# Kernel tuning notes

Measured on AMD Instinct MI355X. Metric: run time of the kernel, lower is better.

## Reference

```python
import jax, jax.numpy as jnp
import numpy as np

B, T, D, K = 8, 2048, 128, 2


def setup_inputs() -> dict:
    key = jax.random.key(0)
    k1, k2 = jax.random.split(key)
    z = jax.random.normal(k1, (B, T, D), dtype=jnp.float32)
    gt_dT = jax.random.normal(k2, (B, T, T, K), dtype=jnp.float32)
    sigma = jnp.ones((K,), dtype=jnp.float32)
    return {"z": z, "gt_dT": gt_dT, "sigma": sigma}


def reference(z, gt_dT, sigma):
    # z: [B,T,D], gt_dT: [B,T,T,K], sigma: [K]
    two_sigma_sq = 2.0 * sigma * sigma                    # [K]
    kernel = jnp.sum(gt_dT * gt_dT / two_sigma_sq, axis=-1)  # [B,T,T]
    w = jnp.exp(-kernel)                                  # [B,T,T]
    z2 = jnp.einsum('btd,btd->bt', z, z)                  # [B,T] squared norms
    w_row_col_sum = jnp.sum(w, axis=2) + jnp.sum(w, axis=1)  # [B,T]
    term1_plus_3 = jnp.einsum('bt,bt->b', z2, w_row_col_sum)  # [B]
    wz = jnp.einsum('bij,bjd->bid', w, z)                 # [B,T,D]
    term2 = jnp.einsum('bid,bid->b', wz, z)               # [B]
    Tn = z.shape[1]
    loss = jnp.mean(term1_plus_3 - 2.0 * term2) / (Tn * Tn)
    return loss
```

## Files before the change

### kernel.cpp

```cpp
#include <hip/hip_runtime.h>


#define T_DIM 2048
#define D_DIM 128
#define B_DIM 8
#define TILE 64
#define NTHREADS 256
#define LDS_STRIDE 136

typedef short s16x8 __attribute__((ext_vector_type(8)));
typedef float f32x4 __attribute__((ext_vector_type(4)));

__device__ __forceinline__ unsigned short f2bf(float x) {
    unsigned int u = __float_as_uint(x);
    u += 0x7fffu + ((u >> 16) & 1u);
    return (unsigned short)(u >> 16);
}

__global__ void patch_loss_zero(float* out) { out[0] = 0.0f; }

__global__ __launch_bounds__(NTHREADS)
void patch_loss_kernel(const float* __restrict__ z,
                       const float* __restrict__ gt,
                       const float* __restrict__ sigma,
                       float* __restrict__ out) {
    __shared__ unsigned short zi[TILE][LDS_STRIDE];
    __shared__ unsigned short zj[TILE][LDS_STRIDE];
    __shared__ float s_tile[TILE][TILE];
    __shared__ float z2i[TILE];
    __shared__ float z2j[TILE];
    __shared__ float red[4];

    const int tid = threadIdx.x;
    const int b  = blockIdx.z;
    const int i0 = blockIdx.y * TILE;
    const int j0 = blockIdx.x * TILE;

    const float s0 = sigma[0], s1 = sigma[1];
    const float a0 = 0.5f / (s0 * s0);
    const float a1 = 0.5f / (s1 * s1);

    const float4* zrow_i = (const float4*)(z + (size_t)(b * T_DIM + i0) * D_DIM);
    const float4* zrow_j = (const float4*)(z + (size_t)(b * T_DIM + j0) * D_DIM);
    #pragma unroll
    for (int k = 0; k < 8; ++k) {
        const int idx = tid + k * NTHREADS;
        const int row = idx >> 5;
        const int c4  = idx & 31;
        float4 vi = zrow_i[row * 32 + c4];
        float4 vj = zrow_j[row * 32 + c4];
        ushort4 pi, pj;
        pi.x = f2bf(vi.x); pi.y = f2bf(vi.y); pi.z = f2bf(vi.z); pi.w = f2bf(vi.w);
        pj.x = f2bf(vj.x); pj.y = f2bf(vj.y); pj.z = f2bf(vj.z); pj.w = f2bf(vj.w);
        *(ushort4*)&zi[row][c4 * 4] = pi;
        *(ushort4*)&zj[row][c4 * 4] = pj;
        float si = vi.x*vi.x + vi.y*vi.y + vi.z*vi.z + vi.w*vi.w;
        float sj = vj.x*vj.x + vj.y*vj.y + vj.z*vj.z + vj.w*vj.w;
        #pragma unroll
        for (int m = 16; m >= 1; m >>= 1) {
            si += __shfl_xor(si, m);
            sj += __shfl_xor(sj, m);
        }
        if ((tid & 31) == 0) { z2i[row] = si; z2j[row] = sj; }
    }
    __syncthreads();

    const int wave = tid >> 6;
    const int lane = tid & 63;
    const int lrow = lane & 15;
    const int lk   = lane >> 4;
    const int m_base = wave * 16;

    f32x4 acc0 = {0.f,0.f,0.f,0.f}, acc1 = {0.f,0.f,0.f,0.f};
    f32x4 acc2 = {0.f,0.f,0.f,0.f}, acc3 = {0.f,0.f,0.f,0.f};
    #pragma unroll
    for (int kk = 0; kk < 4; ++kk) {
        const int co = kk * 32 + lk * 8;
        s16x8 a  = *(const s16x8*)&zi[m_base + lrow][co];
        s16x8 b0 = *(const s16x8*)&zj[ 0 + lrow][co];
        s16x8 b1 = *(const s16x8*)&zj[16 + lrow][co];
        s16x8 b2 = *(const s16x8*)&zj[32 + lrow][co];
        s16x8 b3 = *(const s16x8*)&zj[48 + lrow][co];
        acc0 = __builtin_amdgcn_mfma_f32_16x16x32_bf16(a, b0, acc0, 0, 0, 0);
        acc1 = __builtin_amdgcn_mfma_f32_16x16x32_bf16(a, b1, acc1, 0, 0, 0);
        acc2 = __builtin_amdgcn_mfma_f32_16x16x32_bf16(a, b2, acc2, 0, 0, 0);
        acc3 = __builtin_amdgcn_mfma_f32_16x16x32_bf16(a, b3, acc3, 0, 0, 0);
    }
    #pragma unroll
    for (int r = 0; r < 4; ++r) {
        const int row = m_base + lk * 4 + r;
        s_tile[row][ 0 + lrow] = acc0[r];
        s_tile[row][16 + lrow] = acc1[r];
        s_tile[row][32 + lrow] = acc2[r];
        s_tile[row][48 + lrow] = acc3[r];
    }
    __syncthreads();

    const int jq = tid & 31;
    const int ir = tid >> 5;
    float facc = 0.f;
    #pragma unroll
    for (int it = 0; it < 8; ++it) {
        const int i = ir + it * 8;
        const float4* gp = (const float4*)gt
            + (((size_t)(b * T_DIM + i0 + i) * T_DIM + j0) >> 1) + jq;
        float4 g = *gp;
        const float t0 = g.x*g.x*a0 + g.y*g.y*a1;
        const float t1 = g.z*g.z*a0 + g.w*g.w*a1;
        const float w0 = __expf(-t0);
        const float w1 = __expf(-t1);
        const int jj = jq * 2;
        const float zz = z2i[i];
        const float d0 = zz + z2j[jj]     - 2.f * s_tile[i][jj];
        const float d1 = zz + z2j[jj + 1] - 2.f * s_tile[i][jj + 1];
        facc += w0 * d0 + w1 * d1;
    }

    #pragma unroll
    for (int m = 32; m >= 1; m >>= 1) facc += __shfl_xor(facc, m);
    if (lane == 0) red[wave] = facc;
    __syncthreads();
    if (tid == 0) {
        const float scale = 1.0f / ((float)B_DIM * (float)T_DIM * (float)T_DIM);
        atomicAdd(out, (red[0] + red[1] + red[2] + red[3]) * scale);
    }
}

extern "C" void kernel_launch(void* const* d_in, const int* in_sizes, int n_in,
                              void* d_out, int out_size, void* d_ws, size_t ws_size,
                              hipStream_t stream) {
    const float* z     = (const float*)d_in[0];
    const float* gt    = (const float*)d_in[1];
    const float* sigma = (const float*)d_in[2];
    float* out = (float*)d_out;

    patch_loss_zero<<<1, 1, 0, stream>>>(out);
    dim3 grid(T_DIM / TILE, T_DIM / TILE, B_DIM);
    patch_loss_kernel<<<grid, NTHREADS, 0, stream>>>(z, gt, sigma, out);
}
```

Baseline: 395.0 us.

## Precompute bf16 z and squared norms in a prep kernel, drop LDS staging

Adds a prep kernel that converts z to bf16 and computes the row squared norms once into workspace, so the main kernel no longer redoes this per tile. The main kernel removes LDS staging and the s_tile round trip: each wave computes a 32x32 subtile with MFMA, loading fragments straight from global memory and using the accumulators directly in the epilogue. This removes one __syncthreads and the LDS writes and reads. In exchange, gt is read as float2 per lane in an MFMA-shaped pattern, which gives less coalesced access than the old float4 row reads, and fragments come from global or cache memory instead of LDS.

New measurement: 401.8 us. About the same (+1.7%).

```diff
diff --git a/kernel.cpp b/kernel.cpp
--- a/kernel.cpp
+++ b/kernel.cpp
@@ -4,9 +4,7 @@
 #define T_DIM 2048
 #define D_DIM 128
 #define B_DIM 8
-#define TILE 64
 #define NTHREADS 256
-#define LDS_STRIDE 136
 
 typedef short s16x8 __attribute__((ext_vector_type(8)));
 typedef float f32x4 __attribute__((ext_vector_type(4)));
@@ -17,103 +15,81 @@
     return (unsigned short)(u >> 16);
 }
 
-__global__ void patch_loss_zero(float* out) { out[0] = 0.0f; }
+__global__ __launch_bounds__(NTHREADS)
+void patch_prep(const float* __restrict__ z, unsigned short* __restrict__ zbf,
+                float* __restrict__ z2, float* __restrict__ out) {
+    if (blockIdx.x == 0 && threadIdx.x == 0) out[0] = 0.0f;
+    const int row = blockIdx.x * 8 + (threadIdx.x >> 5);
+    const int c4  = threadIdx.x & 31;
+    float4 v = ((const float4*)(z + (size_t)row * D_DIM))[c4];
+    ushort4 p;
+    p.x = f2bf(v.x); p.y = f2bf(v.y); p.z = f2bf(v.z); p.w = f2bf(v.w);
+    ((ushort4*)(zbf + (size_t)row * D_DIM))[c4] = p;
+    float s = v.x*v.x + v.y*v.y + v.z*v.z + v.w*v.w;
+    #pragma unroll
+    for (int m = 16; m >= 1; m >>= 1) s += __shfl_xor(s, m);
+    if (c4 == 0) z2[row] = s;
+}
 
 __global__ __launch_bounds__(NTHREADS)
-void patch_loss_kernel(const float* __restrict__ z,
-                       const float* __restrict__ gt,
-                       const float* __restrict__ sigma,
-                       float* __restrict__ out) {
-    __shared__ unsigned short zi[TILE][LDS_STRIDE];
-    __shared__ unsigned short zj[TILE][LDS_STRIDE];
-    __shared__ float s_tile[TILE][TILE];
-    __shared__ float z2i[TILE];
-    __shared__ float z2j[TILE];
+void patch_loss_main(const unsigned short* __restrict__ zbf,
+                     const float* __restrict__ z2,
+                     const float* __restrict__ gt,
+                     const float* __restrict__ sigma,
+                     float* __restrict__ out) {
     __shared__ float red[4];
+    const int tid  = threadIdx.x;
+    const int wave = tid >> 6;
+    const int lane = tid & 63;
+    const int c = lane & 15;
+    const int q = lane >> 4;
 
-    const int tid = threadIdx.x;
     const int b  = blockIdx.z;
-    const int i0 = blockIdx.y * TILE;
-    const int j0 = blockIdx.x * TILE;
+    const int i0 = blockIdx.y * 64 + (wave >> 1) * 32;
+    const int j0 = blockIdx.x * 64 + (wave & 1) * 32;
 
     const float s0 = sigma[0], s1 = sigma[1];
     const float a0 = 0.5f / (s0 * s0);
     const float a1 = 0.5f / (s1 * s1);
 
-    const float4* zrow_i = (const float4*)(z + (size_t)(b * T_DIM + i0) * D_DIM);
-    const float4* zrow_j = (const float4*)(z + (size_t)(b * T_DIM + j0) * D_DIM);
-    #pragma unroll
-    for (int k = 0; k < 8; ++k) {
-        const int idx = tid + k * NTHREADS;
-        const int row = idx >> 5;
-        const int c4  = idx & 31;
-        float4 vi = zrow_i[row * 32 + c4];
-        float4 vj = zrow_j[row * 32 + c4];
-        ushort4 pi, pj;
-        pi.x = f2bf(vi.x); pi.y = f2bf(vi.y); pi.z = f2bf(vi.z); pi.w = f2bf(vi.w);
-        pj.x = f2bf(vj.x); pj.y = f2bf(vj.y); pj.z = f2bf(vj.z); pj.w = f2bf(vj.w);
-        *(ushort4*)&zi[row][c4 * 4] = pi;
-        *(ushort4*)&zj[row][c4 * 4] = pj;
-        float si = vi.x*vi.x + vi.y*vi.y + vi.z*vi.z + vi.w*vi.w;
-        float sj = vj.x*vj.x + vj.y*vj.y + vj.z*vj.z + vj.w*vj.w;
-        #pragma unroll
-        for (int m = 16; m >= 1; m >>= 1) {
-            si += __shfl_xor(si, m);
-            sj += __shfl_xor(sj, m);
-        }
-        if ((tid & 31) == 0) { z2i[row] = si; z2j[row] = sj; }
-    }
-    __syncthreads();
+    const unsigned short* zi = zbf + ((size_t)b * T_DIM + i0) * D_DIM;
+    const unsigned short* zj = zbf + ((size_t)b * T_DIM + j0) * D_DIM;
 
-    const int wave = tid >> 6;
-    const int lane = tid & 63;
-    const int lrow = lane & 15;
-    const int lk   = lane >> 4;
-    const int m_base = wave * 16;
-
-    f32x4 acc0 = {0.f,0.f,0.f,0.f}, acc1 = {0.f,0.f,0.f,0.f};
-    f32x4 acc2 = {0.f,0.f,0.f,0.f}, acc3 = {0.f,0.f,0.f,0.f};
+    f32x4 acc[2][2] = {};
     #pragma unroll
     for (int kk = 0; kk < 4; ++kk) {
-        const int co = kk * 32 + lk * 8;
-        s16x8 a  = *(const s16x8*)&zi[m_base + lrow][co];
-        s16x8 b0 = *(const s16x8*)&zj[ 0 + lrow][co];
-        s16x8 b1 = *(const s16x8*)&zj[16 + lrow][co];
-        s16x8 b2 = *(const s16x8*)&zj[32 + lrow][co];
-        s16x8 b3 = *(const s16x8*)&zj[48 + lrow][co];
-        acc0 = __builtin_amdgcn_mfma_f32_16x16x32_bf16(a, b0, acc0, 0, 0, 0);
-        acc1 = __builtin_amdgcn_mfma_f32_16x16x32_bf16(a, b1, acc1, 0, 0, 0);
-        acc2 = __builtin_amdgcn_mfma_f32_16x16x32_bf16(a, b2, acc2, 0, 0, 0);
-        acc3 = __builtin_amdgcn_mfma_f32_16x16x32_bf16(a, b3, acc3, 0, 0, 0);
+        const int co = kk * 32 + q * 8;
+        s16x8 fa0 = *(const s16x8*)(zi + (size_t)(c)      * D_DIM + co);
+        s16x8 fa1 = *(const s16x8*)(zi + (size_t)(16 + c) * D_DIM + co);
+        s16x8 fb0 = *(const s16x8*)(zj + (size_t)(c)      * D_DIM + co);
+        s16x8 fb1 = *(const s16x8*)(zj + (size_t)(16 + c) * D_DIM + co);
+        acc[0][0] = __builtin_amdgcn_mfma_f32_16x16x32_bf16(fa0, fb0, acc[0][0], 0, 0, 0);
+        acc[0][1] = __builtin_amdgcn_mfma_f32_16x16x32_bf16(fa0, fb1, acc[0][1], 0, 0, 0);
+        acc[1][0] = __builtin_amdgcn_mfma_f32_16x16x32_bf16(fa1, fb0, acc[1][0], 0, 0, 0);
+        acc[1][1] = __builtin_amdgcn_mfma_f32_16x16x32_bf16(fa1, fb1, acc[1][1], 0, 0, 0);
     }
+
+    const float z2j0 = z2[(size_t)b * T_DIM + j0 + c];
+    const float z2j1 = z2[(size_t)b * T_DIM + j0 + 16 + c];
+
+    float facc = 0.0f;
     #pragma unroll
-    for (int r = 0; r < 4; ++r) {
-        const int row = m_base + lk * 4 + r;
-        s_tile[row][ 0 + lrow] = acc0[r];
-        s_tile[row][16 + lrow] = acc1[r];
-        s_tile[row][32 + lrow] = acc2[r];
-        s_tile[row][48 + lrow] = acc3[r];
-    }
-    __syncthreads();
-
-    const int jq = tid & 31;
-    const int ir = tid >> 5;
-    float facc = 0.f;
-    #pragma unroll
-    for (int it = 0; it < 8; ++it) {
-        const int i = ir + it * 8;
-        const float4* gp = (const float4*)gt
-            + (((size_t)(b * T_DIM + i0 + i) * T_DIM + j0) >> 1) + jq;
-        float4 g = *gp;
-        const float t0 = g.x*g.x*a0 + g.y*g.y*a1;
-        const float t1 = g.z*g.z*a0 + g.w*g.w*a1;
-        const float w0 = __expf(-t0);
-        const float w1 = __expf(-t1);
-        const int jj = jq * 2;
-        const float zz = z2i[i];
-        const float d0 = zz + z2j[jj]     - 2.f * s_tile[i][jj];
-        const float d1 = zz + z2j[jj + 1] - 2.f * s_tile[i][jj + 1];
-        facc += w0 * d0 + w1 * d1;
+    for (int fi = 0; fi < 2; ++fi) {
+        #pragma unroll
+        for (int r = 0; r < 4; ++r) {
+            const int i = i0 + fi * 16 + q * 4 + r;
+            const float zzi = z2[(size_t)b * T_DIM + i];
+            const float* grow = gt + ((size_t)b * T_DIM + i) * (2 * T_DIM);
+            #pragma unroll
+            for (int fj = 0; fj < 2; ++fj) {
+                const int j = j0 + fj * 16 + c;
+                float2 g = *(const float2*)(grow + (size_t)j * 2);
+                float t = g.x * g.x * a0 + g.y * g.y * a1;
+                float w = __expf(-t);
+                float d = zzi + (fj ? z2j1 : z2j0) - 2.0f * acc[fi][fj][r];
+                facc += w * d;
+            }
+        }
     }
 
     #pragma unroll
@@ -134,7 +110,10 @@
     const float* sigma = (const float*)d_in[2];
     float* out = (float*)d_out;
 
-    patch_loss_zero<<<1, 1, 0, stream>>>(out);
-    dim3 grid(T_DIM / TILE, T_DIM / TILE, B_DIM);
-    patch_loss_kernel<<<grid, NTHREADS, 0, stream>>>(z, gt, sigma, out);
+    unsigned short* zbf = (unsigned short*)d_ws;
+    float* z2 = (float*)((char*)d_ws + (size_t)B_DIM * T_DIM * D_DIM * 2);
+
+    patch_prep<<<(B_DIM * T_DIM) / 8, NTHREADS, 0, stream>>>(z, zbf, z2, out);
+    dim3 grid(T_DIM / 64, T_DIM / 64, B_DIM);
+    patch_loss_main<<<grid, NTHREADS, 0, stream>>>(zbf, z2, gt, sigma, out);
 }
```
